# Kernel tuning notes

Hardware: AMD Instinct MI355X
Metric: run time of the kernel (lower is better)

Reference implementation:

```python
import jax, jax.numpy as jnp
import numpy as np

B, S, CI, E, H, L, V, C = 128, 512, 2, 256, 256, 2, 104, 345


def _gru_dir(x, W_ih, W_hh, b_ih, b_hh):
    # x: [B, S, in]; W_ih: [3H, in]; W_hh: [3H, H]
    h_dim = W_hh.shape[1]
    xp = jnp.einsum('bsi,gi->bsg', x, W_ih) + b_ih  # [B, S, 3H] input gates precomputed

    def step(h, xt):
        gh = h @ W_hh.T + b_hh  # [B, 3H]
        xr, xz, xn = jnp.split(xt, 3, axis=-1)
        hr, hz, hn = jnp.split(gh, 3, axis=-1)
        r = jax.nn.sigmoid(xr + hr)
        z = jax.nn.sigmoid(xz + hz)
        n = jnp.tanh(xn + r * hn)
        h_new = (1.0 - z) * n + z * h
        return h_new, h_new

    h0 = jnp.zeros((x.shape[0], h_dim), x.dtype)
    _, ys = jax.lax.scan(step, h0, jnp.swapaxes(xp, 0, 1))
    return jnp.swapaxes(ys, 0, 1)  # [B, S, H]


def _bigru_layer(x, W_ih, W_hh, b_ih, b_hh):
    # stacked-direction params: leading axis 2 = (fwd, bwd)
    fwd = _gru_dir(x, W_ih[0], W_hh[0], b_ih[0], b_hh[0])
    bwd = _gru_dir(x[:, ::-1], W_ih[1], W_hh[1], b_ih[1], b_hh[1])[:, ::-1]
    return jnp.concatenate([fwd, bwd], axis=-1)  # [B, S, 2H]


def setup_inputs() -> dict:
    key = jax.random.key(0)
    ks = jax.random.split(key, 16)
    k = 1.0 / np.sqrt(H)
    u = lambda kk, shp: jax.random.uniform(kk, shp, jnp.float32, -k, k)
    inp = {
        'coordinate': jax.random.normal(ks[0], (B, S, CI), jnp.float32),
        'flag_bits': jax.random.randint(ks[1], (B, S), 0, V),
        'position_encoding': jax.random.randint(ks[2], (B, S), 0, V),
        'coord_W': u(ks[3], (E, CI)),
        'feat_emb': jax.random.normal(ks[4], (V, E), jnp.float32),
        'W_ih_l0': u(ks[5], (2, 3 * H, E)),
        'W_hh_l0': u(ks[6], (2, 3 * H, H)),
        'b_ih_l0': u(ks[7], (2, 3 * H)),
        'b_hh_l0': u(ks[8], (2, 3 * H)),
        'W_ih_l1': u(ks[9], (2, 3 * H, 2 * H)),
        'W_hh_l1': u(ks[10], (2, 3 * H, H)),
        'b_ih_l1': u(ks[11], (2, 3 * H)),
        'b_hh_l1': u(ks[12], (2, 3 * H)),
        'out_W': u(ks[13], (C, 2 * H)),
        'out_b': u(ks[14], (C,)),
    }
    return inp


def reference(coordinate, flag_bits, position_encoding, coord_W, feat_emb,
              W_ih_l0, W_hh_l0, b_ih_l0, b_hh_l0,
              W_ih_l1, W_hh_l1, b_ih_l1, b_hh_l1, out_W, out_b):
    # embed + sum
    x = jnp.einsum('bsc,ec->bse', coordinate, coord_W) \
        + feat_emb[flag_bits] + feat_emb[position_encoding]
    # 2-layer bidirectional GRU (dropout=0)
    h1 = _bigru_layer(x, W_ih_l0, W_hh_l0, b_ih_l0, b_hh_l0)
    h2 = _bigru_layer(h1, W_ih_l1, W_hh_l1, b_ih_l1, b_hh_l1)
    featur = jnp.concatenate([h2[:, -1, :H], h2[:, -1, H:]], axis=1)  # [B, 2H]
    logits = featur @ out_W.T + out_b  # [B, C]
    return (logits, featur)
```

## Files before the change

### kernel.cpp

```cpp
#include <hip/hip_runtime.h>
#include <stdint.h>

#define B_ 128
#define S_ 512
#define E_ 256
#define H_ 256
#define G3 768
#define C_ 345
#define TC_ 64
#define NCH (S_ / TC_)

typedef __attribute__((ext_vector_type(8))) short short8;
typedef __attribute__((ext_vector_type(4))) float f32x4;
typedef __attribute__((ext_vector_type(4))) unsigned int uint4_;

__device__ __forceinline__ unsigned short f2bf(float f) {
  union { float f; uint32_t u; } v; v.f = f;
  uint32_t r = v.u + 0x7FFF + ((v.u >> 16) & 1);
  return (unsigned short)(r >> 16);
}
__device__ __forceinline__ float bf2f(unsigned short u) {
  union { uint32_t u; float f; } v; v.u = ((uint32_t)u) << 16; return v.f;
}
__device__ __forceinline__ float sigmf(float x) { return 1.f / (1.f + __expf(-x)); }
__device__ __forceinline__ float tanhf_(float x) { return 2.f / (1.f + __expf(-2.f * x)) - 1.f; }

__device__ __forceinline__ void gload_lds16(const void* g, void* l) {
  __builtin_amdgcn_global_load_lds(
      (const __attribute__((address_space(1))) unsigned int*)g,
      (__attribute__((address_space(3))) unsigned int*)l, 16, 0, 0);
}

__global__ void k_sentinel(float* dout) { dout[0] = 1.0e6f; }

__global__ __launch_bounds__(256) void k_cvt(const float* __restrict__ s,
                                             unsigned short* __restrict__ d, int n) {
  int i = blockIdx.x * blockDim.x + threadIdx.x;
  if (i < n) d[i] = f2bf(s[i]);
}

__global__ __launch_bounds__(256) void k_embed_chunk(
    const float* __restrict__ coord, const int* __restrict__ flag,
    const int* __restrict__ pos, const float* __restrict__ cW,
    const float* __restrict__ femb, unsigned short* __restrict__ xeF,
    unsigned short* __restrict__ xeB, int s0) {
  int gid = blockIdx.x * 256 + threadIdx.x;
  int row = gid >> 5, e0 = (gid & 31) * 8;
  int isB = row >= (TC_ * B_);
  int r = isB ? row - TC_ * B_ : row;
  int lt = r >> 7, b = r & 127;
  int t = isB ? (S_ - 1 - (s0 + lt)) : (s0 + lt);
  size_t src = (size_t)b * S_ + t;
  float c0 = coord[src * 2], c1 = coord[src * 2 + 1];
  int f = flag[src], p = pos[src];
  unsigned short* out = (isB ? xeB : xeF) + (size_t)r * E_;
#pragma unroll
  for (int i = 0; i < 8; i++) {
    int e = e0 + i;
    float v = c0 * cW[e * 2] + c1 * cW[e * 2 + 1] + femb[f * E_ + e] + femb[p * E_ + e];
    out[e] = f2bf(v);
  }
}

__global__ __launch_bounds__(256) void k_gemm_bt(
    const unsigned short* __restrict__ A, const unsigned short* __restrict__ Bm,
    unsigned short* __restrict__ C, int M, int N, int K) {
  __shared__ unsigned short As[128 * 32];
  __shared__ unsigned short Bs[128 * 32];
  int nt_ = N >> 7;
  int bx = blockIdx.x % nt_, by = blockIdx.x / nt_;
  int tid = threadIdx.x, lane = tid & 63, w = tid >> 6;
  int wr = (w >> 1) * 64, wc = (w & 1) * 64;
  f32x4 acc[4][4] = {};
  int lr = lane >> 2;
  int lc = (lane & 3) * 8;
  for (int kt = 0; kt < K; kt += 32) {
#pragma unroll
    for (int q = 0; q < 2; q++) {
      int r = w * 32 + q * 16;
      gload_lds16(A + (size_t)(by * 128 + r + lr) * K + kt + lc, &As[r * 32]);
      gload_lds16(Bm + (size_t)(bx * 128 + r + lr) * K + kt + lc, &Bs[r * 32]);
    }
    __syncthreads();
    short8 af[4], bf[4];
#pragma unroll
    for (int i = 0; i < 4; i++)
      af[i] = *(const short8*)&As[(wr + i * 16 + (lane & 15)) * 32 + (lane >> 4) * 8];
#pragma unroll
    for (int i = 0; i < 4; i++)
      bf[i] = *(const short8*)&Bs[(wc + i * 16 + (lane & 15)) * 32 + (lane >> 4) * 8];
#pragma unroll
    for (int i = 0; i < 4; i++)
#pragma unroll
      for (int j = 0; j < 4; j++)
        acc[i][j] = __builtin_amdgcn_mfma_f32_16x16x32_bf16(af[i], bf[j], acc[i][j], 0, 0, 0);
    __syncthreads();
  }
#pragma unroll
  for (int i = 0; i < 4; i++)
#pragma unroll
    for (int j = 0; j < 4; j++)
#pragma unroll
      for (int e = 0; e < 4; e++) {
        int rrow = by * 128 + wr + i * 16 + (lane >> 4) * 4 + e;
        int ccol = bx * 128 + wc + j * 16 + (lane & 15);
        C[(size_t)rrow * N + ccol] = f2bf(acc[i][j][e]);
      }
}

__global__ __launch_bounds__(512) void k_scan_chunk(
    const unsigned short* __restrict__ xpF, const unsigned short* __restrict__ xpB,
    const unsigned short* __restrict__ Whh,
    const float* __restrict__ bih, const float* __restrict__ bhh,
    float* __restrict__ hstate,
    unsigned short* __restrict__ hout,
    int s0, int write_hout) {
  __shared__ __align__(16) char smem[114688];
  char* wlds = smem;
  char* hbf = smem + 65536;
  float* hf32 = (float*)(smem + 65536 + 16384);

  int tid = threadIdx.x, lane = tid & 63, w = tid >> 6;
  int dir = blockIdx.x >> 3;
  int b0 = (blockIdx.x & 7) * 16;

  const unsigned short* Wd = Whh + (size_t)dir * G3 * H_;
  const unsigned short* xq = dir ? xpB : xpF;
  const float* bihd = bih + dir * G3;
  const float* bhhd = bhh + dir * G3;
  float* hst = hstate + (size_t)dir * B_ * H_;

  if (s0 == 0) {
    for (int i = tid; i < 12288; i += 512) ((uint32_t*)hbf)[i] = 0;
  } else {
    for (int i = tid; i < 4096; i += 512) {
      int br = i >> 8, j = i & 255;
      float hv = hst[(size_t)(b0 + br) * H_ + j];
      hf32[br * H_ + j] = hv;
      *(unsigned short*)(hbf + br * 512 + ((j * 2) ^ ((br & 7) << 4))) = f2bf(hv);
    }
  }

  short8 wreg[5][8];
#pragma unroll
  for (int t = 0; t < 5; t++) {
    int grow = (t >> 1) * H_ + 32 * w + (t & 1) * 16 + (lane & 15);
#pragma unroll
    for (int kt = 0; kt < 8; kt++)
      wreg[t][kt] = *(const short8*)&Wd[(size_t)grow * H_ + kt * 32 + (lane >> 4) * 8];
  }
  {
    int base_row = 2 * H_ + 32 * w + 16;
    char* wt = wlds + w * 8192;
    for (int it = 0; it < 8; it++) {
      int r = it * 2 + (lane >> 5);
      int cb = (lane & 31) * 16;
      uint4_ v = *(const uint4_*)&Wd[(size_t)(base_row + r) * H_ + cb / 2];
      *(uint4_*)(wt + r * 512 + (cb ^ ((r & 7) << 4))) = v;
    }
  }
  float brih[2][3], brhh[2][3];
#pragma unroll
  for (int jt = 0; jt < 2; jt++)
#pragma unroll
    for (int g = 0; g < 3; g++) {
      int gg = g * H_ + 32 * w + jt * 16 + (lane & 15);
      brih[jt][g] = bihd[gg];
      brhh[jt][g] = bhhd[gg];
    }
  __syncthreads();

  int p = 0;
  for (int sl = 0; sl < TC_; sl++) {
    int t = dir ? (S_ - 1 - (s0 + sl)) : (s0 + sl);
    f32x4 acc[6] = {};
    char* hb = hbf + p * 8192;
#pragma unroll
    for (int kt = 0; kt < 8; kt++) {
      int ar = lane & 15;
      short8 af = *(const short8*)(hb + ar * 512 + ((kt * 64 + (lane >> 4) * 16) ^ ((ar & 7) << 4)));
#pragma unroll
      for (int t5 = 0; t5 < 5; t5++)
        acc[t5] = __builtin_amdgcn_mfma_f32_16x16x32_bf16(af, wreg[t5][kt], acc[t5], 0, 0, 0);
      short8 bf = *(const short8*)(wlds + w * 8192 + ar * 512 +
                                   ((kt * 64 + (lane >> 4) * 16) ^ ((ar & 7) << 4)));
      acc[5] = __builtin_amdgcn_mfma_f32_16x16x32_bf16(af, bf, acc[5], 0, 0, 0);
    }
    char* hbn = hbf + (p ^ 1) * 8192;
    float* hfp = hf32 + p * 4096;
    float* hfn = hf32 + (p ^ 1) * 4096;
#pragma unroll
    for (int jt = 0; jt < 2; jt++) {
      int j = 32 * w + jt * 16 + (lane & 15);
#pragma unroll
      for (int e = 0; e < 4; e++) {
        int br = (lane >> 4) * 4 + e;
        size_t xbase = ((size_t)sl * B_ + (b0 + br)) * G3;
        float xr = bf2f(xq[xbase + j]) + brih[jt][0];
        float xz = bf2f(xq[xbase + H_ + j]) + brih[jt][1];
        float xn = bf2f(xq[xbase + 2 * H_ + j]) + brih[jt][2];
        float gr = acc[0 + jt][e] + brhh[jt][0];
        float gz = acc[2 + jt][e] + brhh[jt][1];
        float gn = acc[4 + jt][e] + brhh[jt][2];
        float r = sigmf(xr + gr);
        float z = sigmf(xz + gz);
        float n = tanhf_(xn + r * gn);
        float hp = hfp[br * H_ + j];
        float hv = (1.f - z) * n + z * hp;
        hfn[br * H_ + j] = hv;
        unsigned short hb16 = f2bf(hv);
        *(unsigned short*)(hbn + br * 512 + ((j * 2) ^ ((br & 7) << 4))) = hb16;
        if (write_hout)
          hout[((size_t)t * B_ + (b0 + br)) * 512 + dir * H_ + j] = hb16;
      }
    }
    __syncthreads();
    p ^= 1;
  }
  {
    float* hfp = hf32 + p * 4096;
    for (int i = tid; i < 4096; i += 512)
      hst[(size_t)(b0 + (i >> 8)) * H_ + (i & 255)] = hfp[i];
  }
}

__global__ __launch_bounds__(256) void k_final(
    const unsigned short* __restrict__ h1, const float* __restrict__ hlastf,
    const float* __restrict__ Wih1, const float* __restrict__ bih1,
    const float* __restrict__ bhh1, const float* __restrict__ outW,
    const float* __restrict__ outb, float* __restrict__ dout) {
  typedef __attribute__((ext_vector_type(4))) float f4;
  int b = blockIdx.x, tid = threadIdx.x;
  __shared__ float xt[512];
  __shared__ float feat[512];
  for (int i = tid; i < 512; i += 256)
    xt[i] = bf2f(h1[((size_t)(S_ - 1) * B_ + b) * 512 + i]);
  __syncthreads();
  {
    const float* w0 = Wih1 + (size_t)G3 * 512;
    f4 dr = {0.f, 0.f, 0.f, 0.f}, dz = dr, dn = dr;
    const f4* xv = (const f4*)xt;
    const f4* wr_ = (const f4*)(w0 + (size_t)tid * 512);
    const f4* wz_ = (const f4*)(w0 + (size_t)(H_ + tid) * 512);
    const f4* wn_ = (const f4*)(w0 + (size_t)(2 * H_ + tid) * 512);
    for (int k = 0; k < 128; k++) {
      f4 x = xv[k];
      dr += x * wr_[k]; dz += x * wz_[k]; dn += x * wn_[k];
    }
    float sr = dr[0] + dr[1] + dr[2] + dr[3] + bih1[G3 + tid] + bhh1[G3 + tid];
    float sz = dz[0] + dz[1] + dz[2] + dz[3] + bih1[G3 + H_ + tid] + bhh1[G3 + H_ + tid];
    float sn = dn[0] + dn[1] + dn[2] + dn[3] + bih1[G3 + 2 * H_ + tid];
    float r = sigmf(sr);
    float z = sigmf(sz);
    float n = tanhf_(sn + r * bhh1[G3 + 2 * H_ + tid]);
    feat[H_ + tid] = (1.f - z) * n;
    feat[tid] = hlastf[(size_t)b * H_ + tid];
  }
  __syncthreads();
  for (int c = tid; c < C_; c += 256) {
    const f4* wv = (const f4*)(outW + (size_t)c * 512);
    const f4* fv = (const f4*)feat;
    f4 a = {0.f, 0.f, 0.f, 0.f};
    for (int k = 0; k < 128; k++) a += fv[k] * wv[k];
    dout[(size_t)b * C_ + c] = a[0] + a[1] + a[2] + a[3] + outb[c];
  }
  float* fout = dout + (size_t)B_ * C_;
  for (int i = tid; i < 512; i += 256) fout[(size_t)b * 512 + i] = feat[i];
}

extern "C" void kernel_launch(void* const* d_in, const int* in_sizes, int n_in,
                              void* d_out, int out_size, void* d_ws, size_t ws_size,
                              hipStream_t stream) {
  const float* coord = (const float*)d_in[0];
  const int* flag = (const int*)d_in[1];
  const int* pos = (const int*)d_in[2];
  const float* cW = (const float*)d_in[3];
  const float* femb = (const float*)d_in[4];
  const float* Wih0 = (const float*)d_in[5];
  const float* Whh0 = (const float*)d_in[6];
  const float* bih0 = (const float*)d_in[7];
  const float* bhh0 = (const float*)d_in[8];
  const float* Wih1 = (const float*)d_in[9];
  const float* Whh1 = (const float*)d_in[10];
  const float* bih1 = (const float*)d_in[11];
  const float* bhh1 = (const float*)d_in[12];
  const float* outW = (const float*)d_in[13];
  const float* outb = (const float*)d_in[14];
  float* dout = (float*)d_out;

  char* ws = (char*)d_ws;
  size_t off = 0;
  unsigned short* W0b   = (unsigned short*)(ws + off); off += (size_t)2 * G3 * E_ * 2;
  unsigned short* Whh0b = (unsigned short*)(ws + off); off += (size_t)2 * G3 * H_ * 2;
  unsigned short* W1b   = (unsigned short*)(ws + off); off += (size_t)G3 * 512 * 2;
  unsigned short* Whh1b = (unsigned short*)(ws + off); off += (size_t)G3 * H_ * 2;
  float* hstate0        = (float*)(ws + off);          off += (size_t)2 * B_ * H_ * 4;
  float* hstate1        = (float*)(ws + off);          off += (size_t)B_ * H_ * 4;
  unsigned short* xeF   = (unsigned short*)(ws + off); off += (size_t)TC_ * B_ * E_ * 2;
  unsigned short* xeB   = (unsigned short*)(ws + off); off += (size_t)TC_ * B_ * E_ * 2;
  unsigned short* xpF   = (unsigned short*)(ws + off); off += (size_t)TC_ * B_ * G3 * 2;
  unsigned short* xpB   = (unsigned short*)(ws + off); off += (size_t)TC_ * B_ * G3 * 2;
  unsigned short* h1    = (unsigned short*)(ws + off); off += (size_t)S_ * B_ * 512 * 2;

  if (ws_size < off) {
    k_sentinel<<<1, 1, 0, stream>>>(dout);
    return;
  }

  k_cvt<<<(2 * G3 * E_ + 255) / 256, 256, 0, stream>>>(Wih0, W0b, 2 * G3 * E_);
  k_cvt<<<(2 * G3 * H_ + 255) / 256, 256, 0, stream>>>(Whh0, Whh0b, 2 * G3 * H_);
  k_cvt<<<(G3 * 512 + 255) / 256, 256, 0, stream>>>(Wih1, W1b, G3 * 512);
  k_cvt<<<(G3 * H_ + 255) / 256, 256, 0, stream>>>(Whh1, Whh1b, G3 * H_);

  const int MCH = TC_ * B_;
  for (int c = 0; c < NCH; c++) {
    int s0 = c * TC_;
    k_embed_chunk<<<(2 * MCH * 32) / 256, 256, 0, stream>>>(coord, flag, pos, cW, femb,
                                                            xeF, xeB, s0);
    k_gemm_bt<<<(G3 / 128) * (MCH / 128), 256, 0, stream>>>(xeF, W0b, xpF, MCH, G3, E_);
    k_gemm_bt<<<(G3 / 128) * (MCH / 128), 256, 0, stream>>>(xeB, W0b + (size_t)G3 * E_,
                                                            xpB, MCH, G3, E_);
    k_scan_chunk<<<16, 512, 0, stream>>>(xpF, xpB, Whh0b, bih0, bhh0, hstate0, h1, s0, 1);
  }
  for (int c = 0; c < NCH; c++) {
    int s0 = c * TC_;
    k_gemm_bt<<<(G3 / 128) * (MCH / 128), 256, 0, stream>>>(
        h1 + (size_t)s0 * B_ * 512, W1b, xpF, MCH, G3, 512);
    k_scan_chunk<<<8, 512, 0, stream>>>(xpF, xpF, Whh1b, bih1, bhh1, hstate1, nullptr, s0, 0);
  }
  k_final<<<B_, 256, 0, stream>>>(h1, hstate1, Wih1, bih1, bhh1, outW, outb, dout);
}
```

Before: 4.806 ms.

## Prefetch next-step input gates into LDS and keep hidden state in registers

Each timestep of the recurrent scan kernel now issues an async global-to-LDS copy of the next step's precomputed input-gate slice into a double buffer, so those loads overlap the MFMA work instead of sitting on the critical path as scattered global reads. The fp32 hidden state moves from LDS into per-thread registers, which removes an LDS read and write per element each step. The input bias is folded into the projection GEMM epilogue, which drops three adds per element in the scan. In exchange LDS use grows to 128KB and register pressure rises, and the input gates now carry the bias in bf16 rounding.

```diff
diff --git a/kernel.cpp b/kernel.cpp
--- a/kernel.cpp
+++ b/kernel.cpp
@@ -64,7 +64,8 @@
 
 __global__ __launch_bounds__(256) void k_gemm_bt(
     const unsigned short* __restrict__ A, const unsigned short* __restrict__ Bm,
-    unsigned short* __restrict__ C, int M, int N, int K) {
+    unsigned short* __restrict__ C, const float* __restrict__ bias,
+    int M, int N, int K) {
   __shared__ unsigned short As[128 * 32];
   __shared__ unsigned short Bs[128 * 32];
   int nt_ = N >> 7;
@@ -104,21 +105,22 @@
       for (int e = 0; e < 4; e++) {
         int rrow = by * 128 + wr + i * 16 + (lane >> 4) * 4 + e;
         int ccol = bx * 128 + wc + j * 16 + (lane & 15);
-        C[(size_t)rrow * N + ccol] = f2bf(acc[i][j][e]);
+        float v = acc[i][j][e] + (bias ? bias[ccol] : 0.f);
+        C[(size_t)rrow * N + ccol] = f2bf(v);
       }
 }
 
-__global__ __launch_bounds__(512) void k_scan_chunk(
+__global__ __launch_bounds__(512, 2) void k_scan_chunk(
     const unsigned short* __restrict__ xpF, const unsigned short* __restrict__ xpB,
     const unsigned short* __restrict__ Whh,
-    const float* __restrict__ bih, const float* __restrict__ bhh,
+    const float* __restrict__ bhh,
     float* __restrict__ hstate,
     unsigned short* __restrict__ hout,
     int s0, int write_hout) {
-  __shared__ __align__(16) char smem[114688];
+  __shared__ __align__(16) char smem[131072];
   char* wlds = smem;
   char* hbf = smem + 65536;
-  float* hf32 = (float*)(smem + 65536 + 16384);
+  char* xlds = smem + 65536 + 16384;
 
   int tid = threadIdx.x, lane = tid & 63, w = tid >> 6;
   int dir = blockIdx.x >> 3;
@@ -126,18 +128,36 @@
 
   const unsigned short* Wd = Whh + (size_t)dir * G3 * H_;
   const unsigned short* xq = dir ? xpB : xpF;
-  const float* bihd = bih + dir * G3;
   const float* bhhd = bhh + dir * G3;
   float* hst = hstate + (size_t)dir * B_ * H_;
 
+  float hreg[2][4];
+
   if (s0 == 0) {
-    for (int i = tid; i < 12288; i += 512) ((uint32_t*)hbf)[i] = 0;
+    for (int i = tid; i < 4096; i += 512) ((uint32_t*)hbf)[i] = 0;
+#pragma unroll
+    for (int jt = 0; jt < 2; jt++)
+#pragma unroll
+      for (int e = 0; e < 4; e++) hreg[jt][e] = 0.f;
   } else {
-    for (int i = tid; i < 4096; i += 512) {
-      int br = i >> 8, j = i & 255;
-      float hv = hst[(size_t)(b0 + br) * H_ + j];
-      hf32[br * H_ + j] = hv;
-      *(unsigned short*)(hbf + br * 512 + ((j * 2) ^ ((br & 7) << 4))) = f2bf(hv);
+#pragma unroll
+    for (int jt = 0; jt < 2; jt++)
+#pragma unroll
+      for (int e = 0; e < 4; e++) {
+        int j = 32 * w + jt * 16 + (lane & 15);
+        int br = (lane >> 4) * 4 + e;
+        float hv = hst[(size_t)(b0 + br) * H_ + j];
+        hreg[jt][e] = hv;
+        *(unsigned short*)(hbf + br * 512 + ((j * 2) ^ ((br & 7) << 4))) = f2bf(hv);
+      }
+  }
+
+  {
+    const char* gsrc = (const char*)(xq + ((size_t)0 * B_ + b0) * G3);
+#pragma unroll
+    for (int q = 0; q < 3; q++) {
+      int o = (w * 3 + q) * 1024;
+      gload_lds16(gsrc + o + lane * 16, xlds + o);
     }
   }
 
@@ -159,26 +179,33 @@
       *(uint4_*)(wt + r * 512 + (cb ^ ((r & 7) << 4))) = v;
     }
   }
-  float brih[2][3], brhh[2][3];
+  float brhh[2][3];
 #pragma unroll
   for (int jt = 0; jt < 2; jt++)
 #pragma unroll
-    for (int g = 0; g < 3; g++) {
-      int gg = g * H_ + 32 * w + jt * 16 + (lane & 15);
-      brih[jt][g] = bihd[gg];
-      brhh[jt][g] = bhhd[gg];
-    }
+    for (int g = 0; g < 3; g++)
+      brhh[jt][g] = bhhd[g * H_ + 32 * w + jt * 16 + (lane & 15)];
   __syncthreads();
 
   int p = 0;
   for (int sl = 0; sl < TC_; sl++) {
-    int t = dir ? (S_ - 1 - (s0 + sl)) : (s0 + sl);
+    {
+      int sp = (sl + 1 < TC_) ? sl + 1 : sl;
+      const char* gsrc = (const char*)(xq + ((size_t)sp * B_ + b0) * G3);
+      char* ldst = xlds + (p ^ 1) * 24576;
+#pragma unroll
+      for (int q = 0; q < 3; q++) {
+        int o = (w * 3 + q) * 1024;
+        gload_lds16(gsrc + o + lane * 16, ldst + o);
+      }
+    }
     f32x4 acc[6] = {};
     char* hb = hbf + p * 8192;
 #pragma unroll
     for (int kt = 0; kt < 8; kt++) {
       int ar = lane & 15;
-      short8 af = *(const short8*)(hb + ar * 512 + ((kt * 64 + (lane >> 4) * 16) ^ ((ar & 7) << 4)));
+      short8 af = *(const short8*)(hb + ar * 512 +
+                                   ((kt * 64 + (lane >> 4) * 16) ^ ((ar & 7) << 4)));
 #pragma unroll
       for (int t5 = 0; t5 < 5; t5++)
         acc[t5] = __builtin_amdgcn_mfma_f32_16x16x32_bf16(af, wreg[t5][kt], acc[t5], 0, 0, 0);
@@ -186,28 +213,27 @@
                                    ((kt * 64 + (lane >> 4) * 16) ^ ((ar & 7) << 4)));
       acc[5] = __builtin_amdgcn_mfma_f32_16x16x32_bf16(af, bf, acc[5], 0, 0, 0);
     }
+    int t = dir ? (S_ - 1 - (s0 + sl)) : (s0 + sl);
     char* hbn = hbf + (p ^ 1) * 8192;
-    float* hfp = hf32 + p * 4096;
-    float* hfn = hf32 + (p ^ 1) * 4096;
+    const unsigned short* xl = (const unsigned short*)(xlds + p * 24576);
 #pragma unroll
     for (int jt = 0; jt < 2; jt++) {
       int j = 32 * w + jt * 16 + (lane & 15);
 #pragma unroll
       for (int e = 0; e < 4; e++) {
         int br = (lane >> 4) * 4 + e;
-        size_t xbase = ((size_t)sl * B_ + (b0 + br)) * G3;
-        float xr = bf2f(xq[xbase + j]) + brih[jt][0];
-        float xz = bf2f(xq[xbase + H_ + j]) + brih[jt][1];
-        float xn = bf2f(xq[xbase + 2 * H_ + j]) + brih[jt][2];
+        const unsigned short* xr_ = xl + br * G3;
+        float xr = bf2f(xr_[j]);
+        float xz = bf2f(xr_[H_ + j]);
+        float xn = bf2f(xr_[2 * H_ + j]);
         float gr = acc[0 + jt][e] + brhh[jt][0];
         float gz = acc[2 + jt][e] + brhh[jt][1];
         float gn = acc[4 + jt][e] + brhh[jt][2];
         float r = sigmf(xr + gr);
         float z = sigmf(xz + gz);
         float n = tanhf_(xn + r * gn);
-        float hp = hfp[br * H_ + j];
-        float hv = (1.f - z) * n + z * hp;
-        hfn[br * H_ + j] = hv;
+        float hv = (1.f - z) * n + z * hreg[jt][e];
+        hreg[jt][e] = hv;
         unsigned short hb16 = f2bf(hv);
         *(unsigned short*)(hbn + br * 512 + ((j * 2) ^ ((br & 7) << 4))) = hb16;
         if (write_hout)
@@ -217,11 +243,14 @@
     __syncthreads();
     p ^= 1;
   }
-  {
-    float* hfp = hf32 + p * 4096;
-    for (int i = tid; i < 4096; i += 512)
-      hst[(size_t)(b0 + (i >> 8)) * H_ + (i & 255)] = hfp[i];
-  }
+#pragma unroll
+  for (int jt = 0; jt < 2; jt++)
+#pragma unroll
+    for (int e = 0; e < 4; e++) {
+      int j = 32 * w + jt * 16 + (lane & 15);
+      int br = (lane >> 4) * 4 + e;
+      hst[(size_t)(b0 + br) * H_ + j] = hreg[jt][e];
+    }
 }
 
 __global__ __launch_bounds__(256) void k_final(
@@ -317,16 +346,17 @@
     int s0 = c * TC_;
     k_embed_chunk<<<(2 * MCH * 32) / 256, 256, 0, stream>>>(coord, flag, pos, cW, femb,
                                                             xeF, xeB, s0);
-    k_gemm_bt<<<(G3 / 128) * (MCH / 128), 256, 0, stream>>>(xeF, W0b, xpF, MCH, G3, E_);
+    k_gemm_bt<<<(G3 / 128) * (MCH / 128), 256, 0, stream>>>(xeF, W0b, xpF, bih0,
+                                                            MCH, G3, E_);
     k_gemm_bt<<<(G3 / 128) * (MCH / 128), 256, 0, stream>>>(xeB, W0b + (size_t)G3 * E_,
-                                                            xpB, MCH, G3, E_);
-    k_scan_chunk<<<16, 512, 0, stream>>>(xpF, xpB, Whh0b, bih0, bhh0, hstate0, h1, s0, 1);
+                                                            xpB, bih0 + G3, MCH, G3, E_);
+    k_scan_chunk<<<16, 512, 0, stream>>>(xpF, xpB, Whh0b, bhh0, hstate0, h1, s0, 1);
   }
   for (int c = 0; c < NCH; c++) {
     int s0 = c * TC_;
     k_gemm_bt<<<(G3 / 128) * (MCH / 128), 256, 0, stream>>>(
-        h1 + (size_t)s0 * B_ * 512, W1b, xpF, MCH, G3, 512);
-    k_scan_chunk<<<8, 512, 0, stream>>>(xpF, xpF, Whh1b, bih1, bhh1, hstate1, nullptr, s0, 0);
+        h1 + (size_t)s0 * B_ * 512, W1b, xpF, bih1, MCH, G3, 512);
+    k_scan_chunk<<<8, 512, 0, stream>>>(xpF, xpF, Whh1b, bhh1, hstate1, nullptr, s0, 0);
   }
   k_final<<<B_, 256, 0, stream>>>(h1, hstate1, Wih1, bih1, bhh1, outW, outb, dout);
 }
```

Result: faster. 4.269 ms (-11.2%).
